# Kernel optimization log

Measured on AMD Instinct MI355X. Metric: run time of the kernel, lower is better.

## Reference

```python
import jax, jax.numpy as jnp
import numpy as np

B, IN, H = 16384, 1024, 1024


def setup_inputs() -> dict:
    key = jax.random.key(0)
    ks = jax.random.split(key, 7)
    s_in = 1.0 / np.sqrt(IN)
    s_h = 1.0 / np.sqrt(H)
    return {
        "x": jax.random.normal(ks[0], (B, IN), jnp.float32),
        "h0": jax.random.normal(ks[1], (B, H), jnp.float32),
        "c0": jax.random.normal(ks[2], (B, H), jnp.float32),
        # gate order along leading dim: f, i, o, g
        "wi": jax.random.uniform(ks[3], (4, H, IN), jnp.float32, -s_in, s_in),
        "bi": jax.random.uniform(ks[4], (4, H), jnp.float32, -s_in, s_in),
        "wh": jax.random.uniform(ks[5], (4, H, H), jnp.float32, -s_h, s_h),
        "bh": jax.random.uniform(ks[6], (4, H), jnp.float32, -s_h, s_h),
    }


def reference(x, h0, c0, wi, bi, wh, bh):
    # pre-activations for all 4 gates in two fused GEMMs: [b, 4, h]
    z = (jnp.einsum("bi,ghi->bgh", x, wi) + bi
         + jnp.einsum("bj,ghj->bgh", h0, wh) + bh)
    f = jax.nn.sigmoid(z[:, 0])   # forget gate
    i = jax.nn.sigmoid(z[:, 1])   # input gate
    o = jax.nn.sigmoid(z[:, 2])   # output gate
    g = jnp.tanh(z[:, 3])         # candidates
    ct = f * c0 + i * g
    ht = o * jnp.tanh(ct)
    return ht, ct
```

## Files before the change

kernel.cpp:

```cpp
#include <hip/hip_runtime.h>
#include <hip/hip_bf16.h>
#include <stdint.h>

#define B_ROWS 16384
#define K_DIM  2048
#define H_DIM  1024
#define N_DIM  4096
#define KB     (K_DIM * 2)
#define NT     (K_DIM / 64)
#define BUFSZ  65536u

using f32x4  = __attribute__((ext_vector_type(4))) float;
using bf16x8 = __attribute__((ext_vector_type(8))) __bf16;

__device__ __forceinline__ unsigned short f2bf(float f) {
    union { float f; unsigned u; } v; v.f = f;
    unsigned r = v.u + 0x7fffu + ((v.u >> 16) & 1u);
    return (unsigned short)(r >> 16);
}

__device__ __forceinline__ void gload16(const void* g, const void* l) {
    __builtin_amdgcn_global_load_lds(
        (const __attribute__((address_space(1))) void*)g,
        (__attribute__((address_space(3))) void*)l,
        16, 0, 0);
}

__device__ __forceinline__ float rcp1p(float e) {
    return __builtin_amdgcn_rcpf(1.f + e);
}

__global__ void pack_a_kernel(const float* __restrict__ x, const float* __restrict__ h0,
                              unsigned short* __restrict__ A) {
    int tid = blockIdx.x * 256 + threadIdx.x;
    int64_t idx = (int64_t)tid * 4;
    int b = (int)(idx >> 11);
    int k = (int)(idx & 2047);
    const float* src = (k < 1024) ? (x + (int64_t)b * 1024 + k)
                                  : (h0 + (int64_t)b * 1024 + (k - 1024));
    float4 v = *(const float4*)src;
    ushort4 o;
    o.x = f2bf(v.x); o.y = f2bf(v.y); o.z = f2bf(v.z); o.w = f2bf(v.w);
    *(ushort4*)(A + idx) = o;
}

__global__ void pack_w_kernel(const float* __restrict__ wi, const float* __restrict__ wh,
                              const float* __restrict__ bi, const float* __restrict__ bh,
                              unsigned short* __restrict__ W, float* __restrict__ bias) {
    int tid = blockIdx.x * 256 + threadIdx.x;
    int64_t idx = (int64_t)tid * 4;
    int r = (int)(idx >> 11);
    int k = (int)(idx & 2047);
    int h = r >> 2, g = r & 3;
    const float* src = (k < 1024)
        ? (wi + (int64_t)g * 1048576 + (int64_t)h * 1024 + k)
        : (wh + (int64_t)g * 1048576 + (int64_t)h * 1024 + (k - 1024));
    float4 v = *(const float4*)src;
    ushort4 o;
    o.x = f2bf(v.x); o.y = f2bf(v.y); o.z = f2bf(v.z); o.w = f2bf(v.w);
    *(ushort4*)(W + idx) = o;
    if (k == 0) bias[r] = bi[g * 1024 + h] + bh[g * 1024 + h];
}


#define FENCE   asm volatile("" ::: "memory")
#define SCHED0  __builtin_amdgcn_sched_barrier(0)
#define BAR     __builtin_amdgcn_s_barrier()

#define PH_PRE  do { FENCE; BAR; \
                     asm volatile("s_waitcnt lgkmcnt(0)" ::: "memory"); \
                     SCHED0; __builtin_amdgcn_s_setprio(1); } while (0)
#define PH_POST do { __builtin_amdgcn_s_setprio(0); SCHED0; FENCE; BAR; } while (0)
#define PH_POST_V do { __builtin_amdgcn_s_setprio(0); SCHED0; \
                       asm volatile("s_waitcnt vmcnt(6)" ::: "memory"); \
                       SCHED0; FENCE; BAR; } while (0)

__global__ __launch_bounds__(512, 2) void lstm_gemm_fused(
    const unsigned short* __restrict__ A, const unsigned short* __restrict__ W,
    const float* __restrict__ bias, const float* __restrict__ c0,
    float* __restrict__ ht, float* __restrict__ ct)
{
    __shared__ char sm[131072];

    const int tid = threadIdx.x;
    const int l   = tid & 63;
    const int w   = tid >> 6;
    const int wm  = w >> 2;
    const int wn  = w & 3;

    const int bid = blockIdx.x;
    const int nid = (bid & 7) * 128 + (bid >> 3);
    const int bm  = nid >> 4;
    const int bn  = nid & 15;

    f32x4 acc[8][4];
#pragma unroll
    for (int i = 0; i < 8; ++i)
#pragma unroll
        for (int j = 0; j < 4; ++j) acc[i][j] = (f32x4){0.f, 0.f, 0.f, 0.f};

    const int srow = w * 16 + (l >> 2);
    const int scb  = ((l & 3) << 4) ^ (l & 32);
    const char* Asrc = (const char*)A + (size_t)(bm * 256 + srow) * KB + scb;
    const char* Wsrc = (const char*)W + (size_t)(bn * 256 + srow) * KB + scb;
    const uint32_t AstL = (uint32_t)w * 1024u;
    const uint32_t BstL = 32768u + (uint32_t)w * 1024u;

#define STAGE_A(TS, H, BOFF) do { \
    const char* s_ = Asrc + (size_t)(TS) * 128 + (H) * 64; \
    gload16(s_,            sm + (BOFF) + (H) * 16384u + AstL); \
    gload16(s_ + 128 * KB, sm + (BOFF) + (H) * 16384u + 8192u + AstL); \
} while (0)
#define STAGE_B(TS, H, BOFF) do { \
    const char* s_ = Wsrc + (size_t)(TS) * 128 + (H) * 64; \
    gload16(s_,            sm + (BOFF) + (H) * 16384u + BstL); \
    gload16(s_ + 128 * KB, sm + (BOFF) + (H) * 16384u + 8192u + BstL); \
} while (0)

    const int rr = l & 15, kg = l >> 4;
    const uint32_t loff = (uint32_t)rr * 64u + (((uint32_t)kg * 16u) ^ (uint32_t)((rr & 8) << 2));
    const uint32_t Ard = (uint32_t)(wm * 8) * 1024u + loff;
    const uint32_t Brd = 32768u + (uint32_t)(wn * 4) * 1024u + loff;

    bf16x8 a[8], b0, b1;

#define LOAD_A(BOFF, KK) do { \
    _Pragma("unroll") \
    for (int mf_ = 0; mf_ < 8; ++mf_) \
        a[mf_] = *(const bf16x8*)(sm + (BOFF) + (KK) * 16384u + Ard + mf_ * 1024u); \
} while (0)
#define RD_B(BOFF, KK, NF) (*(const bf16x8*)(sm + (BOFF) + (KK) * 16384u + Brd + (NF) * 1024u))
#define MM2(NF0, NF1) do { \
    _Pragma("unroll") \
    for (int mf_ = 0; mf_ < 8; ++mf_) { \
        acc[mf_][NF0] = __builtin_amdgcn_mfma_f32_16x16x32_bf16(a[mf_], b0, acc[mf_][NF0], 0, 0, 0); \
        acc[mf_][NF1] = __builtin_amdgcn_mfma_f32_16x16x32_bf16(a[mf_], b1, acc[mf_][NF1], 0, 0, 0); \
    } \
} while (0)

    STAGE_A(0, 0, 0u); STAGE_B(0, 0, 0u); STAGE_A(0, 1, 0u); STAGE_B(0, 1, 0u);
    STAGE_A(1, 0, BUFSZ); STAGE_B(1, 0, BUFSZ); STAGE_A(1, 1, BUFSZ);
    asm volatile("s_waitcnt vmcnt(6)" ::: "memory");
    SCHED0; FENCE; BAR;

#define DO_TILE(CUR, NXT, T) do { \
    const int tn1_ = ((T) + 1 < NT) ? (T) + 1 : NT - 1; \
    const int tn2_ = ((T) + 2 < NT) ? (T) + 2 : NT - 1; \
     \
    LOAD_A(CUR, 0); \
    b0 = RD_B(CUR, 0, 0); b1 = RD_B(CUR, 0, 1); \
    STAGE_B(tn1_, 1, NXT); \
    PH_PRE; MM2(0, 1); PH_POST; \
     \
    b0 = RD_B(CUR, 0, 2); b1 = RD_B(CUR, 0, 3); \
    STAGE_A(tn2_, 0, CUR); \
    PH_PRE; MM2(2, 3); PH_POST; \
     \
    LOAD_A(CUR, 1); \
    b0 = RD_B(CUR, 1, 0); b1 = RD_B(CUR, 1, 1); \
    STAGE_B(tn2_, 0, CUR); \
    PH_PRE; MM2(0, 1); PH_POST; \
     \
    b0 = RD_B(CUR, 1, 2); b1 = RD_B(CUR, 1, 3); \
    STAGE_A(tn2_, 1, CUR); \
    PH_PRE; MM2(2, 3); PH_POST_V; \
} while (0)

#pragma unroll 1
    for (int tt = 0; tt < NT; tt += 2) {
        DO_TILE(0u, BUFSZ, tt);
        DO_TILE(BUFSZ, 0u, tt + 1);
    }

    asm volatile("s_waitcnt vmcnt(0)" ::: "memory");
    FENCE; BAR;

    float* ep = (float*)(void*)sm + w * 1088;
    const int hbase = bn * 64 + wn * 16;
    const int rbase = bm * 256 + wm * 128;

#pragma unroll
    for (int mf = 0; mf < 8; ++mf) {
#pragma unroll
        for (int nf = 0; nf < 4; ++nf)
#pragma unroll
            for (int r = 0; r < 4; ++r)
                ep[((l >> 4) * 4 + r) * 68 + nf * 16 + (l & 15)] = acc[mf][nf][r];

#pragma unroll
        for (int it = 0; it < 4; ++it) {
            const int row = (l >> 4) + it * 4;
            const int hs  = l & 15;
            f32x4 z = *(const f32x4*)(ep + row * 68 + hs * 4);
            const int hg = hbase + hs;
            const float4 bz = ((const float4*)bias)[hg];
            const int brow = rbase + mf * 16 + row;

            float zf = z.x + bz.x;
            float zi = z.y + bz.y;
            float zo = z.z + bz.z;
            float zg = z.w + bz.w;

            float fg = rcp1p(__expf(-zf));
            float ig = rcp1p(__expf(-zi));
            float og = rcp1p(__expf(-zo));
            float gg = 2.f * rcp1p(__expf(-2.f * zg)) - 1.f;

            int64_t oi = (int64_t)brow * H_DIM + hg;
            float c  = fg * c0[oi] + ig * gg;
            float hh = og * (2.f * rcp1p(__expf(-2.f * c)) - 1.f);
            ct[oi] = c;
            ht[oi] = hh;
        }
    }
}

extern "C" void kernel_launch(void* const* d_in, const int* in_sizes, int n_in,
                              void* d_out, int out_size, void* d_ws, size_t ws_size,
                              hipStream_t stream) {
    const float* x  = (const float*)d_in[0];
    const float* h0 = (const float*)d_in[1];
    const float* c0 = (const float*)d_in[2];
    const float* wi = (const float*)d_in[3];
    const float* bi = (const float*)d_in[4];
    const float* wh = (const float*)d_in[5];
    const float* bh = (const float*)d_in[6];

    float* ht = (float*)d_out;
    float* ct = ht + (int64_t)B_ROWS * H_DIM;

    char* ws = (char*)d_ws;
    unsigned short* A  = (unsigned short*)ws;
    unsigned short* Wp = (unsigned short*)(ws + (64u << 20));
    float*          bs = (float*)(ws + (80u << 20));

    pack_a_kernel<<<32768, 256, 0, stream>>>(x, h0, A);
    pack_w_kernel<<<8192, 256, 0, stream>>>(wi, wh, bi, bh, Wp, bs);

    lstm_gemm_fused<<<1024, 512, 0, stream>>>(A, Wp, bs, c0, ht, ct);
}
```

Baseline: 312.0 us.

## Restructure GEMM main loop into single-tile-ahead prefetch with 4x4 MFMA phases

The main loop is rescheduled. Instead of prefetching two tiles ahead, half-tiles of A and B into the current buffer, it now stages only the next tile into the other buffer. Each phase loads four A fragments and all four B fragments, then issues a 4x4 block of MFMAs. This raises LDS fragment reuse per phase and reduces prefetch depth and vmcnt waits (6→4). It also simplifies the buffer hazards, but the shallower prefetch distance may expose global load latency.

Result: no change. 311.0 us (-0.3%).

```diff
diff --git a/kernel.cpp b/kernel.cpp
--- a/kernel.cpp
+++ b/kernel.cpp
@@ -63,8 +63,8 @@
 }
 
 
+#define SCHED0  __builtin_amdgcn_sched_barrier(0)
 #define FENCE   asm volatile("" ::: "memory")
-#define SCHED0  __builtin_amdgcn_sched_barrier(0)
 #define BAR     __builtin_amdgcn_s_barrier()
 
 #define PH_PRE  do { FENCE; BAR; \
@@ -72,7 +72,7 @@
                      SCHED0; __builtin_amdgcn_s_setprio(1); } while (0)
 #define PH_POST do { __builtin_amdgcn_s_setprio(0); SCHED0; FENCE; BAR; } while (0)
 #define PH_POST_V do { __builtin_amdgcn_s_setprio(0); SCHED0; \
-                       asm volatile("s_waitcnt vmcnt(6)" ::: "memory"); \
+                       asm volatile("s_waitcnt vmcnt(4)" ::: "memory"); \
                        SCHED0; FENCE; BAR; } while (0)
 
 __global__ __launch_bounds__(512, 2) void lstm_gemm_fused(
@@ -103,67 +103,69 @@
     const int scb  = ((l & 3) << 4) ^ (l & 32);
     const char* Asrc = (const char*)A + (size_t)(bm * 256 + srow) * KB + scb;
     const char* Wsrc = (const char*)W + (size_t)(bn * 256 + srow) * KB + scb;
-    const uint32_t AstL = (uint32_t)w * 1024u;
-    const uint32_t BstL = 32768u + (uint32_t)w * 1024u;
-
-#define STAGE_A(TS, H, BOFF) do { \
-    const char* s_ = Asrc + (size_t)(TS) * 128 + (H) * 64; \
-    gload16(s_,            sm + (BOFF) + (H) * 16384u + AstL); \
-    gload16(s_ + 128 * KB, sm + (BOFF) + (H) * 16384u + 8192u + AstL); \
-} while (0)
-#define STAGE_B(TS, H, BOFF) do { \
-    const char* s_ = Wsrc + (size_t)(TS) * 128 + (H) * 64; \
-    gload16(s_,            sm + (BOFF) + (H) * 16384u + BstL); \
-    gload16(s_ + 128 * KB, sm + (BOFF) + (H) * 16384u + 8192u + BstL); \
+    const uint32_t wL = (uint32_t)w * 1024u;
+
+#define STAGE_A(TS, KK, BOFF) do { \
+    const char* s_ = Asrc + (size_t)(TS) * 128 + (KK) * 64; \
+    gload16(s_,            sm + (BOFF) + (KK) * 16384u + wL); \
+    gload16(s_ + 128 * KB, sm + (BOFF) + (KK) * 16384u + 8192u + wL); \
+} while (0)
+#define STAGE_B(TS, KK, BOFF) do { \
+    const char* s_ = Wsrc + (size_t)(TS) * 128 + (KK) * 64; \
+    gload16(s_,            sm + (BOFF) + 32768u + (KK) * 16384u + wL); \
+    gload16(s_ + 128 * KB, sm + (BOFF) + 32768u + (KK) * 16384u + 8192u + wL); \
 } while (0)
 
     const int rr = l & 15, kg = l >> 4;
     const uint32_t loff = (uint32_t)rr * 64u + (((uint32_t)kg * 16u) ^ (uint32_t)((rr & 8) << 2));
-    const uint32_t Ard = (uint32_t)(wm * 8) * 1024u + loff;
-    const uint32_t Brd = 32768u + (uint32_t)(wn * 4) * 1024u + loff;
-
-    bf16x8 a[8], b0, b1;
-
-#define LOAD_A(BOFF, KK) do { \
+    const uint32_t Ard = (uint32_t)wm * 8192u + loff;
+    const uint32_t Brd = 32768u + (uint32_t)wn * 4096u + loff;
+
+    bf16x8 aL[4], aH[4], bb[4];
+
+#define RD_A4(BOFF, KK, MB, ARR) do { \
     _Pragma("unroll") \
-    for (int mf_ = 0; mf_ < 8; ++mf_) \
-        a[mf_] = *(const bf16x8*)(sm + (BOFF) + (KK) * 16384u + Ard + mf_ * 1024u); \
-} while (0)
-#define RD_B(BOFF, KK, NF) (*(const bf16x8*)(sm + (BOFF) + (KK) * 16384u + Brd + (NF) * 1024u))
-#define MM2(NF0, NF1) do { \
+    for (int i_ = 0; i_ < 4; ++i_) \
+        ARR[i_] = *(const bf16x8*)(sm + (BOFF) + (KK) * 16384u + Ard + ((MB) + i_) * 1024u); \
+} while (0)
+#define RD_B4(BOFF, KK) do { \
     _Pragma("unroll") \
-    for (int mf_ = 0; mf_ < 8; ++mf_) { \
-        acc[mf_][NF0] = __builtin_amdgcn_mfma_f32_16x16x32_bf16(a[mf_], b0, acc[mf_][NF0], 0, 0, 0); \
-        acc[mf_][NF1] = __builtin_amdgcn_mfma_f32_16x16x32_bf16(a[mf_], b1, acc[mf_][NF1], 0, 0, 0); \
-    } \
-} while (0)
-
-    STAGE_A(0, 0, 0u); STAGE_B(0, 0, 0u); STAGE_A(0, 1, 0u); STAGE_B(0, 1, 0u);
-    STAGE_A(1, 0, BUFSZ); STAGE_B(1, 0, BUFSZ); STAGE_A(1, 1, BUFSZ);
-    asm volatile("s_waitcnt vmcnt(6)" ::: "memory");
+    for (int i_ = 0; i_ < 4; ++i_) \
+        bb[i_] = *(const bf16x8*)(sm + (BOFF) + (KK) * 16384u + Brd + i_ * 1024u); \
+} while (0)
+
+#define MFMA16H(ARR, MB) do { \
+    _Pragma("unroll") \
+    for (int mf_ = 0; mf_ < 4; ++mf_) \
+        _Pragma("unroll") \
+        for (int nf_ = 0; nf_ < 4; ++nf_) \
+            acc[(MB) + mf_][nf_] = __builtin_amdgcn_mfma_f32_16x16x32_bf16( \
+                ARR[mf_], bb[nf_], acc[(MB) + mf_][nf_], 0, 0, 0); \
+} while (0)
+
+    STAGE_A(0, 0, 0u); STAGE_B(0, 0, 0u);
+    STAGE_A(0, 1, 0u); STAGE_B(0, 1, 0u);
+    asm volatile("s_waitcnt vmcnt(4)" ::: "memory");
     SCHED0; FENCE; BAR;
 
 #define DO_TILE(CUR, NXT, T) do { \
-    const int tn1_ = ((T) + 1 < NT) ? (T) + 1 : NT - 1; \
-    const int tn2_ = ((T) + 2 < NT) ? (T) + 2 : NT - 1; \
-     \
-    LOAD_A(CUR, 0); \
-    b0 = RD_B(CUR, 0, 0); b1 = RD_B(CUR, 0, 1); \
-    STAGE_B(tn1_, 1, NXT); \
-    PH_PRE; MM2(0, 1); PH_POST; \
-     \
-    b0 = RD_B(CUR, 0, 2); b1 = RD_B(CUR, 0, 3); \
-    STAGE_A(tn2_, 0, CUR); \
-    PH_PRE; MM2(2, 3); PH_POST; \
-     \
-    LOAD_A(CUR, 1); \
-    b0 = RD_B(CUR, 1, 0); b1 = RD_B(CUR, 1, 1); \
-    STAGE_B(tn2_, 0, CUR); \
-    PH_PRE; MM2(0, 1); PH_POST; \
-     \
-    b0 = RD_B(CUR, 1, 2); b1 = RD_B(CUR, 1, 3); \
-    STAGE_A(tn2_, 1, CUR); \
-    PH_PRE; MM2(2, 3); PH_POST_V; \
+    const int st_ = ((T) + 1 < NT) ? (T) + 1 : NT - 1; \
+     \
+    RD_A4(CUR, 0, 0, aL); RD_B4(CUR, 0); \
+    STAGE_A(st_, 0, NXT); \
+    PH_PRE; MFMA16H(aL, 0); PH_POST; \
+     \
+    RD_A4(CUR, 0, 4, aH); \
+    STAGE_B(st_, 0, NXT); \
+    PH_PRE; MFMA16H(aH, 4); PH_POST_V; \
+     \
+    RD_A4(CUR, 1, 0, aL); RD_B4(CUR, 1); \
+    STAGE_A(st_, 1, NXT); \
+    PH_PRE; MFMA16H(aL, 0); PH_POST; \
+     \
+    RD_A4(CUR, 1, 4, aH); \
+    STAGE_B(st_, 1, NXT); \
+    PH_PRE; MFMA16H(aH, 4); PH_POST_V; \
 } while (0)
 
 #pragma unroll 1
@@ -172,7 +174,7 @@
         DO_TILE(BUFSZ, 0u, tt + 1);
     }
 
-    asm volatile("s_waitcnt vmcnt(0)" ::: "memory");
+    asm volatile("s_waitcnt vmcnt(0) lgkmcnt(0)" ::: "memory");
     FENCE; BAR;
 
     float* ep = (float*)(void*)sm + w * 1088;
```
